# Kernel optimization log

Hardware: AMD Instinct MI355X
Metric: run time of the kernel (lower is better)

Reference implementation:

```python
import jax, jax.numpy as jnp
import numpy as np

VOXEL_SIZE = 0.04
M = 32768            # voxels surviving from previous level
V = 9                # views per fragment
C = 24               # image feature channels at finest scale
H, W = 120, 160      # fine feature map size (640x480 images /4)
C_PRE = 50           # channels[1] + tsdf + occ from previous level
UP_OFFSETS = np.array([[0,0,0,0],[0,1,0,0],[0,0,1,0],[0,0,0,1],
                       [0,1,1,0],[0,1,0,1],[0,0,1,1],[0,1,1,1]], dtype=np.int32)


def setup_inputs():
    key = jax.random.key(0)
    ks = jax.random.split(key, 10)
    pre_feat = jax.random.normal(ks[0], (M, C_PRE), jnp.float32)
    xyz = jax.random.randint(ks[1], (M, 3), 0, 94).astype(jnp.int32)
    pre_coords = jnp.concatenate([jnp.zeros((M, 1), jnp.int32), xyz], axis=1)
    feats = jax.random.normal(ks[2], (V, 1, C, H, W), jnp.float32)
    # plausible pinhole KRcam = K @ [R|t], identity rotation, jittered translation
    fx = fy = 100.0
    cx, cy = (W - 1) / 2.0, (H - 1) / 2.0
    K = np.array([[fx, 0, cx, 0], [0, fy, cy, 0], [0, 0, 1, 0], [0, 0, 0, 1]], np.float32)
    t = np.asarray(jax.random.uniform(ks[3], (V, 3), minval=-0.2, maxval=0.2))
    RT = np.tile(np.eye(4, dtype=np.float32), (V, 1, 1))
    RT[:, :3, 3] = t
    KRcam = jnp.asarray(np.einsum('ij,vjk->vik', K, RT).astype(np.float32))[:, None]  # (V,1,4,4)
    vol_origin = jnp.array([[-1.9, -1.9, 0.5]], jnp.float32)
    w2ac = jnp.asarray(np.eye(4, dtype=np.float32)[None]) + 0.01 * jax.random.normal(ks[4], (1, 4, 4), jnp.float32)
    W_sp = jax.random.normal(ks[5], (C + 1 + C_PRE, 24), jnp.float32) * 0.1
    b_sp = jnp.zeros((24,), jnp.float32)
    W_t = jax.random.normal(ks[6], (24, 1), jnp.float32) * 0.1
    b_t = jnp.zeros((1,), jnp.float32)
    W_o = jax.random.normal(ks[7], (24, 1), jnp.float32) * 0.1
    b_o = jnp.zeros((1,), jnp.float32)
    return dict(pre_feat=pre_feat, pre_coords=pre_coords, feats=feats, KRcam=KRcam,
                vol_origin=vol_origin, world_to_aligned_camera=w2ac,
                W_sp=W_sp, b_sp=b_sp, W_t=W_t, b_t=b_t, W_o=W_o, b_o=b_o)


def upsample(pre_feat, pre_coords, interval):
    # 1 -> 8 octree coordinate upsample (NeuConHead.upsample)
    off = jnp.asarray(UP_OFFSETS) * interval          # batch col stays 0
    up_coords = (pre_coords[:, None, :] + off[None]).reshape(-1, 4)
    up_feat = jnp.broadcast_to(pre_feat[:, None, :], (pre_feat.shape[0], 8, pre_feat.shape[1])).reshape(-1, pre_feat.shape[1])
    return up_feat, up_coords


def back_project(coords_xyz, origin, voxel_size, feats, KRcam):
    # coords_xyz: (N,3) int voxel coords; feats: (V,C,H,W); KRcam: (V,4,4)
    n = coords_xyz.shape[0]
    world = coords_xyz.astype(jnp.float32) * voxel_size + origin          # (N,3)
    homog = jnp.concatenate([world, jnp.ones((n, 1), jnp.float32)], 1)    # (N,4)
    im_p = jnp.einsum('vij,nj->vin', KRcam, homog)                        # (V,4,N)
    im_x, im_y, im_z = im_p[:, 0], im_p[:, 1], im_p[:, 2]
    safe_z = jnp.where(jnp.abs(im_z) > 1e-9, im_z, 1e-9)
    px = im_x / safe_z
    py = im_y / safe_z
    mask = (px >= 0) & (px <= W - 1) & (py >= 0) & (py <= H - 1) & (im_z > 0)  # (V,N)

    def sample_view(img, x, y, m):
        # bilinear grid_sample, align_corners=True, zero padding; img (C,H,W)
        x0 = jnp.floor(x); y0 = jnp.floor(y)
        wx = x - x0; wy = y - y0
        def gather(xi, yi):
            ok = (xi >= 0) & (xi < W) & (yi >= 0) & (yi < H)
            v = img[:, jnp.clip(yi, 0, H - 1).astype(jnp.int32), jnp.clip(xi, 0, W - 1).astype(jnp.int32)]
            return v * ok  # (C,N)
        top = gather(x0, y0) * (1 - wx) + gather(x0 + 1, y0) * wx
        bot = gather(x0, y0 + 1) * (1 - wx) + gather(x0 + 1, y0 + 1) * wx
        return jnp.where(m, top * (1 - wy) + bot * wy, 0.0)  # (C,N)

    fsamp = jax.vmap(sample_view)(feats, px, py, mask)        # (V,C,N)
    zed = jnp.where(mask, im_z, 0.0)                          # (V,N)
    count = mask.sum(0).astype(jnp.float32)                   # (N,)
    denom = jnp.maximum(count, 1.0)
    features = fsamp.sum(0) / denom                           # (C,N)
    z = zed.sum(0) / denom                                    # (N,)
    pos = z > 0
    npos = jnp.maximum(pos.sum(), 1).astype(jnp.float32)
    zmean = jnp.where(pos, z, 0.0).sum() / npos
    znorm = jnp.sqrt(jnp.where(pos, (z - zmean) ** 2, 0.0).sum()) + 1e-5  # torch.norm
    zn = jnp.where(pos, (z - zmean) / znorm, 0.0)
    volume = jnp.concatenate([features.T, zn[:, None]], axis=1)  # (N, C+1)
    return volume, count


def reference(pre_feat, feats, KRcam, vol_origin, world_to_aligned_camera,
              W_sp, b_sp, W_t, b_t, W_o, b_o, pre_coords):
    up_feat, up_coords = upsample(pre_feat, pre_coords, 1)
    volume, count = back_project(up_coords[:, 1:], vol_origin[0], VOXEL_SIZE,
                                 feats[:, 0], KRcam[:, 0])
    feat = jnp.concatenate([volume, up_feat], axis=1)          # (N, 75)
    # r_coords: world -> aligned camera frame (bs=1)
    world = up_coords[:, 1:].astype(jnp.float32) * VOXEL_SIZE + vol_origin[0]
    homog = jnp.concatenate([world, jnp.ones_like(world[:, :1])], axis=1)
    cam = homog @ world_to_aligned_camera[0, :3, :].T          # (N,3)
    r_coords = jnp.concatenate([cam, up_coords[:, :1].astype(jnp.float32)], axis=1)
    h = jax.nn.relu(feat @ W_sp + b_sp)                        # SPVCNN stand-in head
    tsdf = h @ W_t + b_t
    occ = h @ W_o + b_o
    out = jnp.concatenate([tsdf, occ], axis=1)                 # (N,2)
    return out, count, r_coords
```

## Files before the change

### kernel.cpp

```cpp
#include <hip/hip_runtime.h>
#include <hip/hip_fp16.h>

#define Mpts 32768
#define Vv 9
#define Cc 24
#define Hh 120
#define Ww 160
#define Npts (Mpts * 8)
#define PIX (Hh * Ww)
#define VOXEL 0.04f

#define NSLOT 64

#define OFF_TF    (NSLOT * 64)
#define OFF_PREH  (OFF_TF + Vv * PIX * 32)
#define OFF_HP    (OFF_PREH + Mpts * Cc * 4)
#define OFF_Z     (OFF_HP + Npts * Cc * 2)

typedef __attribute__((ext_vector_type(2))) float f32x2;
typedef __attribute__((ext_vector_type(4))) float f32x4;
typedef __attribute__((ext_vector_type(4))) int i32x4;

__device__ __forceinline__ unsigned pack2h(float a, float b) {
  __half2 h = __floats2half2_rn(a, b);
  return *(unsigned*)&h;
}

__device__ __forceinline__ unsigned pack4fp8(float a, float b, float c,
                                             float d) {
  int u = __builtin_amdgcn_cvt_pk_fp8_f32(a, b, 0, false);
  u = __builtin_amdgcn_cvt_pk_fp8_f32(c, d, u, true);
  return (unsigned)u;
}

__global__ __launch_bounds__(256) void prep_kernel(
    const float* __restrict__ feats, const float* __restrict__ pre_feat,
    const float* __restrict__ W_sp, const float* __restrict__ b_sp,
    uint4* __restrict__ tf, float* __restrict__ pre_h,
    double* __restrict__ red) {
  __shared__ float tile[64][Cc + 1];
  __shared__ float Wl[50 * Cc];
  __shared__ float bl[Cc];
  int blk = blockIdx.x;
  if (blk == 0) {
    red[threadIdx.x] = 0.0;
    red[threadIdx.x + 256] = 0.0;
  }

  if (blk < Vv * 300) {
    int v = blk / 300;
    int p0 = (blk % 300) * 64;
    const float* src = feats + (size_t)v * (Cc * PIX);
    for (int i = threadIdx.x; i < Cc * 64; i += 256) {
      int c = i >> 6, p = i & 63;
      tile[p][c] = src[c * PIX + p0 + p];
    }
    __syncthreads();
    uint4* dst = tf + ((size_t)v * PIX + p0) * 2;
    if (threadIdx.x < 128) {
      int p = threadIdx.x >> 1, sel = threadIdx.x & 1;
      const float* t = &tile[p][0];
      uint4 u;
      if (sel == 0) {
        u.x = pack4fp8(t[0], t[1], t[2], t[3]);
        u.y = pack4fp8(t[4], t[5], t[6], t[7]);
        u.z = pack4fp8(t[8], t[9], t[10], t[11]);
        u.w = pack4fp8(t[12], t[13], t[14], t[15]);
      } else {
        u.x = pack4fp8(t[16], t[17], t[18], t[19]);
        u.y = pack4fp8(t[20], t[21], t[22], t[23]);
        u.z = 0;
        u.w = 0;
      }
      dst[p * 2 + sel] = u;
    }
  } else {
    int mb = blk - Vv * 300;
    for (int i = threadIdx.x; i < 50 * Cc; i += 256) Wl[i] = W_sp[25 * Cc + i];
    if (threadIdx.x < Cc) bl[threadIdx.x] = b_sp[threadIdx.x];
    __syncthreads();
    int m = mb * 256 + threadIdx.x;
    float acc[Cc];
#pragma unroll
    for (int j = 0; j < Cc; j++) acc[j] = bl[j];
    const f32x2* pf = (const f32x2*)(pre_feat + (size_t)m * 50);
#pragma unroll 5
    for (int k = 0; k < 25; k++) {
      f32x2 x = __builtin_nontemporal_load(pf + k);
#pragma unroll
      for (int j = 0; j < Cc; j++)
        acc[j] += x.x * Wl[(2 * k) * Cc + j] + x.y * Wl[(2 * k + 1) * Cc + j];
    }
    f32x4* o4 = (f32x4*)(pre_h + (size_t)m * Cc);
#pragma unroll
    for (int t = 0; t < 6; t++) {
      f32x4 v4 = {acc[4 * t], acc[4 * t + 1], acc[4 * t + 2], acc[4 * t + 3]};
      __builtin_nontemporal_store(v4, o4 + t);
    }
  }
}

__device__ __forceinline__ void acc16(uint4 A, float w, float* acc) {
#pragma unroll
  for (int t = 0; t < 4; t++) {
    unsigned u = ((const unsigned*)&A)[t];
    f32x2 f0 = __builtin_amdgcn_cvt_pk_f32_fp8((int)u, false);
    f32x2 f1 = __builtin_amdgcn_cvt_pk_f32_fp8((int)u, true);
    acc[4 * t + 0] += w * f0.x;
    acc[4 * t + 1] += w * f0.y;
    acc[4 * t + 2] += w * f1.x;
    acc[4 * t + 3] += w * f1.y;
  }
}
__device__ __forceinline__ void acc8v(unsigned ux, unsigned uy, float w,
                                      float* acc) {
  f32x2 f0 = __builtin_amdgcn_cvt_pk_f32_fp8((int)ux, false);
  f32x2 f1 = __builtin_amdgcn_cvt_pk_f32_fp8((int)ux, true);
  f32x2 f2 = __builtin_amdgcn_cvt_pk_f32_fp8((int)uy, false);
  f32x2 f3 = __builtin_amdgcn_cvt_pk_f32_fp8((int)uy, true);
  acc[0] += w * f0.x;
  acc[1] += w * f0.y;
  acc[2] += w * f1.x;
  acc[3] += w * f1.y;
  acc[4] += w * f2.x;
  acc[5] += w * f2.y;
  acc[6] += w * f3.x;
  acc[7] += w * f3.y;
}

__global__ __launch_bounds__(256) void main_kernel(
    const int* __restrict__ pre_coords, const uint4* __restrict__ tfq,
    const float* __restrict__ KRcam, const float* __restrict__ vol_origin,
    const float* __restrict__ w2ac, const float* __restrict__ W_sp,
    const float* __restrict__ pre_h, float* __restrict__ out,
    unsigned* __restrict__ hp, float* __restrict__ zbuf,
    double* __restrict__ red) {
  __shared__ float KR[Vv * 12];
  __shared__ float w2a[12];
  __shared__ float orig[3];
  __shared__ float redl[3][4];
  for (int i = threadIdx.x; i < Vv * 12; i += 256) {
    int v = i / 12, r = i - v * 12;
    KR[i] = KRcam[v * 16 + r];
  }
  if (threadIdx.x < 12) w2a[threadIdx.x] = w2ac[threadIdx.x];
  if (threadIdx.x < 3) orig[threadIdx.x] = vol_origin[threadIdx.x];
  __syncthreads();

  int n = blockIdx.x * 256 + threadIdx.x;
  int m = n >> 3, o = n & 7;
  i32x4 pc = __builtin_nontemporal_load((const i32x4*)pre_coords + m);
  int cx = pc.y + ((0xB2 >> o) & 1);
  int cy = pc.z + ((0xD4 >> o) & 1);
  int cz = pc.w + ((0xE8 >> o) & 1);
  float wx0 = (float)cx * VOXEL + orig[0];
  float wy0 = (float)cy * VOXEL + orig[1];
  float wz0 = (float)cz * VOXEL + orig[2];

  {
    float camx = w2a[0] * wx0 + w2a[1] * wy0 + w2a[2] * wz0 + w2a[3];
    float camy = w2a[4] * wx0 + w2a[5] * wy0 + w2a[6] * wz0 + w2a[7];
    float camz = w2a[8] * wx0 + w2a[9] * wy0 + w2a[10] * wz0 + w2a[11];
    f32x4 rc = {camx, camy, camz, (float)pc.x};
    __builtin_nontemporal_store(rc, (f32x4*)(out + 3 * (size_t)Npts) + n);
  }

  float acc[Cc];
#pragma unroll
  for (int c = 0; c < Cc; c++) acc[c] = 0.f;
  float zsum = 0.f;
  int cnt = 0;

  for (int v = 0; v < Vv; v++) {
    const float* kr = &KR[v * 12];
    float ix = kr[0] * wx0 + kr[1] * wy0 + kr[2] * wz0 + kr[3];
    float iy = kr[4] * wx0 + kr[5] * wy0 + kr[6] * wz0 + kr[7];
    float iz = kr[8] * wx0 + kr[9] * wy0 + kr[10] * wz0 + kr[11];
    float sz = (fabsf(iz) > 1e-9f) ? iz : 1e-9f;
    float px = ix / sz;
    float py = iy / sz;
    bool msk = (px >= 0.f) && (px <= (float)(Ww - 1)) && (py >= 0.f) &&
               (py <= (float)(Hh - 1)) && (iz > 0.f);
    if (msk) {
      int x0 = (int)floorf(px), y0 = (int)floorf(py);
      int xs = min(x0, Ww - 2), ys = min(y0, Hh - 2);
      float wx = px - (float)xs, wy = py - (float)ys;
      float w00 = (1.f - wx) * (1.f - wy);
      float w10 = wx * (1.f - wy);
      float w01 = (1.f - wx) * wy;
      float w11 = wx * wy;
      const uint4* p = tfq + ((size_t)(v * PIX + ys * Ww + xs)) * 2;
      const uint4* q = p + Ww * 2;
      uint4 A = p[0], B = p[2], C = q[0], D = q[2];
      uint2 Ab = *(const uint2*)(p + 1), Bb = *(const uint2*)(p + 3);
      uint2 Cb = *(const uint2*)(q + 1), Db = *(const uint2*)(q + 3);
      acc16(A, w00, &acc[0]);
      acc8v(Ab.x, Ab.y, w00, &acc[16]);
      acc16(B, w10, &acc[0]);
      acc8v(Bb.x, Bb.y, w10, &acc[16]);
      acc16(C, w01, &acc[0]);
      acc8v(Cb.x, Cb.y, w01, &acc[16]);
      acc16(D, w11, &acc[0]);
      acc8v(Db.x, Db.y, w11, &acc[16]);
      zsum += iz;
      cnt++;
    }
  }

  float denom = fmaxf((float)cnt, 1.f);
  float invd = 1.f / denom;
  float z = zsum * invd;

  float h[Cc];
  {
    const f32x4* ph4 = (const f32x4*)(pre_h + (size_t)m * Cc);
#pragma unroll
    for (int t = 0; t < 6; t++) {
      f32x4 v4 = __builtin_nontemporal_load(ph4 + t);
      h[4 * t + 0] = v4.x;
      h[4 * t + 1] = v4.y;
      h[4 * t + 2] = v4.z;
      h[4 * t + 3] = v4.w;
    }
  }
#pragma unroll
  for (int c = 0; c < Cc; c++) {
    float f = acc[c] * invd;
#pragma unroll
    for (int j = 0; j < Cc; j++) h[j] += f * W_sp[c * Cc + j];
  }
#pragma unroll
  for (int j2 = 0; j2 < 12; j2++)
    __builtin_nontemporal_store(pack2h(h[2 * j2], h[2 * j2 + 1]),
                                hp + (size_t)j2 * Npts + n);

  __builtin_nontemporal_store(z, zbuf + n);
  __builtin_nontemporal_store((float)cnt, out + 2 * (size_t)Npts + n);

  float rz = (z > 0.f) ? z : 0.f;
  float rz2 = rz * rz;
  float rcn = (z > 0.f) ? 1.f : 0.f;
#pragma unroll
  for (int off = 32; off > 0; off >>= 1) {
    rz += __shfl_down(rz, off);
    rz2 += __shfl_down(rz2, off);
    rcn += __shfl_down(rcn, off);
  }
  int wid = threadIdx.x >> 6, lid = threadIdx.x & 63;
  if (lid == 0) {
    redl[0][wid] = rz;
    redl[1][wid] = rz2;
    redl[2][wid] = rcn;
  }
  __syncthreads();
  if (threadIdx.x == 0) {
    float a = 0.f, b = 0.f, c = 0.f;
#pragma unroll
    for (int w = 0; w < 4; w++) {
      a += redl[0][w];
      b += redl[1][w];
      c += redl[2][w];
    }
    double* slot = red + (size_t)(blockIdx.x & (NSLOT - 1)) * 8;
    atomicAdd(&slot[0], (double)a);
    atomicAdd(&slot[1], (double)b);
    atomicAdd(&slot[2], (double)c);
  }
}

__global__ __launch_bounds__(256) void final_kernel(
    const float* __restrict__ zbuf, const unsigned* __restrict__ hp,
    const float* __restrict__ W_sp, const float* __restrict__ W_t,
    const float* __restrict__ b_t, const float* __restrict__ W_o,
    const float* __restrict__ b_o, const double* __restrict__ red,
    float* __restrict__ out) {
  __shared__ float wz[Cc], wt[Cc], wo[Cc];
  __shared__ float bt, bo, s_zmean, s_izn;
  if (threadIdx.x < Cc) {
    wz[threadIdx.x] = W_sp[24 * Cc + threadIdx.x];
    wt[threadIdx.x] = W_t[threadIdx.x];
    wo[threadIdx.x] = W_o[threadIdx.x];
  }
  if (threadIdx.x == 64) {
    bt = b_t[0];
    bo = b_o[0];
  }
  if (threadIdx.x < NSLOT) {
    double a = red[(size_t)threadIdx.x * 8 + 0];
    double b = red[(size_t)threadIdx.x * 8 + 1];
    double c = red[(size_t)threadIdx.x * 8 + 2];
#pragma unroll
    for (int off = 32; off > 0; off >>= 1) {
      a += __shfl_down(a, off);
      b += __shfl_down(b, off);
      c += __shfl_down(c, off);
    }
    if (threadIdx.x == 0) {
      double npos = (c > 0.0) ? c : 1.0;
      double zmean = a / npos;
      double var = b - 2.0 * zmean * a + c * zmean * zmean;
      if (var < 0.0) var = 0.0;
      double znorm = sqrt(var) + 1e-5;
      s_zmean = (float)zmean;
      s_izn = (float)(1.0 / znorm);
    }
  }
  __syncthreads();
  int n = blockIdx.x * 256 + threadIdx.x;
  float z = __builtin_nontemporal_load(zbuf + n);
  float zn = (z > 0.f) ? (z - s_zmean) * s_izn : 0.f;
  float tsdf = bt, occ = bo;
#pragma unroll
  for (int j2 = 0; j2 < 12; j2++) {
    unsigned u = __builtin_nontemporal_load(hp + (size_t)j2 * Npts + n);
    float2 f = __half22float2(*(const __half2*)&u);
    float h0 = fmaxf(f.x + zn * wz[2 * j2], 0.f);
    float h1 = fmaxf(f.y + zn * wz[2 * j2 + 1], 0.f);
    tsdf += h0 * wt[2 * j2] + h1 * wt[2 * j2 + 1];
    occ += h0 * wo[2 * j2] + h1 * wo[2 * j2 + 1];
  }
  f32x2 o2 = {tsdf, occ};
  __builtin_nontemporal_store(o2, (f32x2*)out + n);
}

extern "C" void kernel_launch(void* const* d_in, const int* in_sizes, int n_in,
                              void* d_out, int out_size, void* d_ws,
                              size_t ws_size, hipStream_t stream) {
  const float* pre_feat = (const float*)d_in[0];
  const int* pre_coords = (const int*)d_in[1];
  const float* feats = (const float*)d_in[2];
  const float* KRcam = (const float*)d_in[3];
  const float* vol_origin = (const float*)d_in[4];
  const float* w2ac = (const float*)d_in[5];
  const float* W_sp = (const float*)d_in[6];
  const float* b_sp = (const float*)d_in[7];
  const float* W_t = (const float*)d_in[8];
  const float* b_t = (const float*)d_in[9];
  const float* W_o = (const float*)d_in[10];
  const float* b_o = (const float*)d_in[11];

  float* out = (float*)d_out;
  char* ws = (char*)d_ws;
  double* red = (double*)ws;
  uint4* tf = (uint4*)(ws + OFF_TF);
  float* pre_h = (float*)(ws + OFF_PREH);
  unsigned* hp = (unsigned*)(ws + OFF_HP);
  float* zbuf = (float*)(ws + OFF_Z);

  prep_kernel<<<Vv * 300 + Mpts / 256, 256, 0, stream>>>(feats, pre_feat, W_sp,
                                                         b_sp, tf, pre_h, red);
  main_kernel<<<Npts / 256, 256, 0, stream>>>(pre_coords, tf, KRcam,
                                              vol_origin, w2ac, W_sp, pre_h,
                                              out, hp, zbuf, red);
  final_kernel<<<Npts / 256, 256, 0, stream>>>(zbuf, hp, W_sp, W_t, b_t, W_o,
                                               b_o, red, out);
}
```

Before: 144.2 us.

## Precompute depth statistics in prep kernel and fuse final head into main kernel

```diff
diff --git a/kernel.cpp b/kernel.cpp
--- a/kernel.cpp
+++ b/kernel.cpp
@@ -10,21 +10,16 @@
 #define PIX (Hh * Ww)
 #define VOXEL 0.04f
 
-#define NSLOT 64
-
-#define OFF_TF    (NSLOT * 64)
+#define NB_TF   (Vv * 300)
+#define NB_GEMM (Mpts / 256)
+#define NB_Z    (Npts / 256)
+
+#define OFF_TF    32768
 #define OFF_PREH  (OFF_TF + Vv * PIX * 32)
-#define OFF_HP    (OFF_PREH + Mpts * Cc * 4)
-#define OFF_Z     (OFF_HP + Npts * Cc * 2)
 
 typedef __attribute__((ext_vector_type(2))) float f32x2;
 typedef __attribute__((ext_vector_type(4))) float f32x4;
 typedef __attribute__((ext_vector_type(4))) int i32x4;
-
-__device__ __forceinline__ unsigned pack2h(float a, float b) {
-  __half2 h = __floats2half2_rn(a, b);
-  return *(unsigned*)&h;
-}
 
 __device__ __forceinline__ unsigned pack4fp8(float a, float b, float c,
                                              float d) {
@@ -36,24 +31,24 @@
 __global__ __launch_bounds__(256) void prep_kernel(
     const float* __restrict__ feats, const float* __restrict__ pre_feat,
     const float* __restrict__ W_sp, const float* __restrict__ b_sp,
-    uint4* __restrict__ tf, float* __restrict__ pre_h,
-    double* __restrict__ red) {
+    const int* __restrict__ pre_coords, const float* __restrict__ KRcam,
+    const float* __restrict__ vol_origin, uint4* __restrict__ tf,
+    float* __restrict__ pre_h, double* __restrict__ red) {
   __shared__ float tile[64][Cc + 1];
   __shared__ float Wl[50 * Cc];
   __shared__ float bl[Cc];
+  __shared__ float KRs[Vv * 12];
+  __shared__ float origs[3];
+  __shared__ float redl[3][4];
   int blk = blockIdx.x;
-  if (blk == 0) {
-    red[threadIdx.x] = 0.0;
-    red[threadIdx.x + 256] = 0.0;
-  }
-
-  if (blk < Vv * 300) {
+
+  if (blk < NB_TF) {
     int v = blk / 300;
     int p0 = (blk % 300) * 64;
     const float* src = feats + (size_t)v * (Cc * PIX);
     for (int i = threadIdx.x; i < Cc * 64; i += 256) {
       int c = i >> 6, p = i & 63;
-      tile[p][c] = src[c * PIX + p0 + p];
+      tile[p][c] = __builtin_nontemporal_load(src + c * PIX + p0 + p);
     }
     __syncthreads();
     uint4* dst = tf + ((size_t)v * PIX + p0) * 2;
@@ -74,8 +69,8 @@
       }
       dst[p * 2 + sel] = u;
     }
-  } else {
-    int mb = blk - Vv * 300;
+  } else if (blk < NB_TF + NB_GEMM) {
+    int mb = blk - NB_TF;
     for (int i = threadIdx.x; i < 50 * Cc; i += 256) Wl[i] = W_sp[25 * Cc + i];
     if (threadIdx.x < Cc) bl[threadIdx.x] = b_sp[threadIdx.x];
     __syncthreads();
@@ -95,7 +90,72 @@
 #pragma unroll
     for (int t = 0; t < 6; t++) {
       f32x4 v4 = {acc[4 * t], acc[4 * t + 1], acc[4 * t + 2], acc[4 * t + 3]};
-      __builtin_nontemporal_store(v4, o4 + t);
+      o4[t] = v4;
+    }
+  } else {
+    int zblk = blk - (NB_TF + NB_GEMM);
+    for (int i = threadIdx.x; i < Vv * 12; i += 256) {
+      int v = i / 12, r = i - v * 12;
+      KRs[i] = KRcam[v * 16 + r];
+    }
+    if (threadIdx.x < 3) origs[threadIdx.x] = vol_origin[threadIdx.x];
+    __syncthreads();
+    int n = zblk * 256 + threadIdx.x;
+    int m = n >> 3, o = n & 7;
+    i32x4 pc = __builtin_nontemporal_load((const i32x4*)pre_coords + m);
+    int cx = pc.y + ((0xB2 >> o) & 1);
+    int cy = pc.z + ((0xD4 >> o) & 1);
+    int cz = pc.w + ((0xE8 >> o) & 1);
+    float wx0 = (float)cx * VOXEL + origs[0];
+    float wy0 = (float)cy * VOXEL + origs[1];
+    float wz0 = (float)cz * VOXEL + origs[2];
+    float zsum = 0.f;
+    int cnt = 0;
+    for (int v = 0; v < Vv; v++) {
+      const float* kr = &KRs[v * 12];
+      float ix = kr[0] * wx0 + kr[1] * wy0 + kr[2] * wz0 + kr[3];
+      float iy = kr[4] * wx0 + kr[5] * wy0 + kr[6] * wz0 + kr[7];
+      float iz = kr[8] * wx0 + kr[9] * wy0 + kr[10] * wz0 + kr[11];
+      float sz = (fabsf(iz) > 1e-9f) ? iz : 1e-9f;
+      float px = ix / sz;
+      float py = iy / sz;
+      bool msk = (px >= 0.f) && (px <= (float)(Ww - 1)) && (py >= 0.f) &&
+                 (py <= (float)(Hh - 1)) && (iz > 0.f);
+      if (msk) {
+        zsum += iz;
+        cnt++;
+      }
+    }
+    float denom = fmaxf((float)cnt, 1.f);
+    float z = zsum / denom;
+    float rz = (z > 0.f) ? z : 0.f;
+    float rz2 = rz * rz;
+    float rcn = (z > 0.f) ? 1.f : 0.f;
+#pragma unroll
+    for (int off = 32; off > 0; off >>= 1) {
+      rz += __shfl_down(rz, off);
+      rz2 += __shfl_down(rz2, off);
+      rcn += __shfl_down(rcn, off);
+    }
+    int wid = threadIdx.x >> 6, lid = threadIdx.x & 63;
+    if (lid == 0) {
+      redl[0][wid] = rz;
+      redl[1][wid] = rz2;
+      redl[2][wid] = rcn;
+    }
+    __syncthreads();
+    if (threadIdx.x == 0) {
+      float a = 0.f, b = 0.f, c = 0.f;
+#pragma unroll
+      for (int w = 0; w < 4; w++) {
+        a += redl[0][w];
+        b += redl[1][w];
+        c += redl[2][w];
+      }
+      double* r3 = red + (size_t)zblk * 3;
+      r3[0] = (double)a;
+      r3[1] = (double)b;
+      r3[2] = (double)c;
     }
   }
 }
@@ -132,19 +192,60 @@
     const int* __restrict__ pre_coords, const uint4* __restrict__ tfq,
     const float* __restrict__ KRcam, const float* __restrict__ vol_origin,
     const float* __restrict__ w2ac, const float* __restrict__ W_sp,
+    const float* __restrict__ W_t, const float* __restrict__ b_t,
+    const float* __restrict__ W_o, const float* __restrict__ b_o,
     const float* __restrict__ pre_h, float* __restrict__ out,
-    unsigned* __restrict__ hp, float* __restrict__ zbuf,
-    double* __restrict__ red) {
+    const double* __restrict__ red) {
   __shared__ float KR[Vv * 12];
   __shared__ float w2a[12];
   __shared__ float orig[3];
-  __shared__ float redl[3][4];
+  __shared__ double dredl[3][4];
+  __shared__ float s_zmean, s_izn;
   for (int i = threadIdx.x; i < Vv * 12; i += 256) {
     int v = i / 12, r = i - v * 12;
     KR[i] = KRcam[v * 16 + r];
   }
   if (threadIdx.x < 12) w2a[threadIdx.x] = w2ac[threadIdx.x];
   if (threadIdx.x < 3) orig[threadIdx.x] = vol_origin[threadIdx.x];
+
+  {
+    double a = 0.0, b = 0.0, c = 0.0;
+    for (int s = threadIdx.x; s < NB_Z; s += 256) {
+      const double* r3 = red + (size_t)s * 3;
+      a += r3[0];
+      b += r3[1];
+      c += r3[2];
+    }
+#pragma unroll
+    for (int off = 32; off > 0; off >>= 1) {
+      a += __shfl_down(a, off);
+      b += __shfl_down(b, off);
+      c += __shfl_down(c, off);
+    }
+    int wid = threadIdx.x >> 6, lid = threadIdx.x & 63;
+    if (lid == 0) {
+      dredl[0][wid] = a;
+      dredl[1][wid] = b;
+      dredl[2][wid] = c;
+    }
+    __syncthreads();
+    if (threadIdx.x == 0) {
+      double A = 0.0, B = 0.0, C = 0.0;
+#pragma unroll
+      for (int w = 0; w < 4; w++) {
+        A += dredl[0][w];
+        B += dredl[1][w];
+        C += dredl[2][w];
+      }
+      double npos = (C > 0.0) ? C : 1.0;
+      double zmean = A / npos;
+      double var = B - 2.0 * zmean * A + C * zmean * zmean;
+      if (var < 0.0) var = 0.0;
+      double znorm = sqrt(var) + 1e-5;
+      s_zmean = (float)zmean;
+      s_izn = (float)(1.0 / znorm);
+    }
+  }
   __syncthreads();
 
   int n = blockIdx.x * 256 + threadIdx.x;
@@ -216,7 +317,7 @@
     const f32x4* ph4 = (const f32x4*)(pre_h + (size_t)m * Cc);
 #pragma unroll
     for (int t = 0; t < 6; t++) {
-      f32x4 v4 = __builtin_nontemporal_load(ph4 + t);
+      f32x4 v4 = ph4[t];
       h[4 * t + 0] = v4.x;
       h[4 * t + 1] = v4.y;
       h[4 * t + 2] = v4.z;
@@ -229,98 +330,18 @@
 #pragma unroll
     for (int j = 0; j < Cc; j++) h[j] += f * W_sp[c * Cc + j];
   }
-#pragma unroll
-  for (int j2 = 0; j2 < 12; j2++)
-    __builtin_nontemporal_store(pack2h(h[2 * j2], h[2 * j2 + 1]),
-                                hp + (size_t)j2 * Npts + n);
-
-  __builtin_nontemporal_store(z, zbuf + n);
-  __builtin_nontemporal_store((float)cnt, out + 2 * (size_t)Npts + n);
-
-  float rz = (z > 0.f) ? z : 0.f;
-  float rz2 = rz * rz;
-  float rcn = (z > 0.f) ? 1.f : 0.f;
-#pragma unroll
-  for (int off = 32; off > 0; off >>= 1) {
-    rz += __shfl_down(rz, off);
-    rz2 += __shfl_down(rz2, off);
-    rcn += __shfl_down(rcn, off);
-  }
-  int wid = threadIdx.x >> 6, lid = threadIdx.x & 63;
-  if (lid == 0) {
-    redl[0][wid] = rz;
-    redl[1][wid] = rz2;
-    redl[2][wid] = rcn;
-  }
-  __syncthreads();
-  if (threadIdx.x == 0) {
-    float a = 0.f, b = 0.f, c = 0.f;
-#pragma unroll
-    for (int w = 0; w < 4; w++) {
-      a += redl[0][w];
-      b += redl[1][w];
-      c += redl[2][w];
-    }
-    double* slot = red + (size_t)(blockIdx.x & (NSLOT - 1)) * 8;
-    atomicAdd(&slot[0], (double)a);
-    atomicAdd(&slot[1], (double)b);
-    atomicAdd(&slot[2], (double)c);
-  }
-}
-
-__global__ __launch_bounds__(256) void final_kernel(
-    const float* __restrict__ zbuf, const unsigned* __restrict__ hp,
-    const float* __restrict__ W_sp, const float* __restrict__ W_t,
-    const float* __restrict__ b_t, const float* __restrict__ W_o,
-    const float* __restrict__ b_o, const double* __restrict__ red,
-    float* __restrict__ out) {
-  __shared__ float wz[Cc], wt[Cc], wo[Cc];
-  __shared__ float bt, bo, s_zmean, s_izn;
-  if (threadIdx.x < Cc) {
-    wz[threadIdx.x] = W_sp[24 * Cc + threadIdx.x];
-    wt[threadIdx.x] = W_t[threadIdx.x];
-    wo[threadIdx.x] = W_o[threadIdx.x];
-  }
-  if (threadIdx.x == 64) {
-    bt = b_t[0];
-    bo = b_o[0];
-  }
-  if (threadIdx.x < NSLOT) {
-    double a = red[(size_t)threadIdx.x * 8 + 0];
-    double b = red[(size_t)threadIdx.x * 8 + 1];
-    double c = red[(size_t)threadIdx.x * 8 + 2];
-#pragma unroll
-    for (int off = 32; off > 0; off >>= 1) {
-      a += __shfl_down(a, off);
-      b += __shfl_down(b, off);
-      c += __shfl_down(c, off);
-    }
-    if (threadIdx.x == 0) {
-      double npos = (c > 0.0) ? c : 1.0;
-      double zmean = a / npos;
-      double var = b - 2.0 * zmean * a + c * zmean * zmean;
-      if (var < 0.0) var = 0.0;
-      double znorm = sqrt(var) + 1e-5;
-      s_zmean = (float)zmean;
-      s_izn = (float)(1.0 / znorm);
-    }
-  }
-  __syncthreads();
-  int n = blockIdx.x * 256 + threadIdx.x;
-  float z = __builtin_nontemporal_load(zbuf + n);
+
   float zn = (z > 0.f) ? (z - s_zmean) * s_izn : 0.f;
-  float tsdf = bt, occ = bo;
-#pragma unroll
-  for (int j2 = 0; j2 < 12; j2++) {
-    unsigned u = __builtin_nontemporal_load(hp + (size_t)j2 * Npts + n);
-    float2 f = __half22float2(*(const __half2*)&u);
-    float h0 = fmaxf(f.x + zn * wz[2 * j2], 0.f);
-    float h1 = fmaxf(f.y + zn * wz[2 * j2 + 1], 0.f);
-    tsdf += h0 * wt[2 * j2] + h1 * wt[2 * j2 + 1];
-    occ += h0 * wo[2 * j2] + h1 * wo[2 * j2 + 1];
+  float tsdf = b_t[0], occ = b_o[0];
+#pragma unroll
+  for (int j = 0; j < Cc; j++) {
+    float hj = fmaxf(h[j] + zn * W_sp[24 * Cc + j], 0.f);
+    tsdf += hj * W_t[j];
+    occ += hj * W_o[j];
   }
   f32x2 o2 = {tsdf, occ};
   __builtin_nontemporal_store(o2, (f32x2*)out + n);
+  __builtin_nontemporal_store((float)cnt, out + 2 * (size_t)Npts + n);
 }
 
 extern "C" void kernel_launch(void* const* d_in, const int* in_sizes, int n_in,
@@ -344,14 +365,11 @@
   double* red = (double*)ws;
   uint4* tf = (uint4*)(ws + OFF_TF);
   float* pre_h = (float*)(ws + OFF_PREH);
-  unsigned* hp = (unsigned*)(ws + OFF_HP);
-  float* zbuf = (float*)(ws + OFF_Z);
-
-  prep_kernel<<<Vv * 300 + Mpts / 256, 256, 0, stream>>>(feats, pre_feat, W_sp,
-                                                         b_sp, tf, pre_h, red);
-  main_kernel<<<Npts / 256, 256, 0, stream>>>(pre_coords, tf, KRcam,
-                                              vol_origin, w2ac, W_sp, pre_h,
-                                              out, hp, zbuf, red);
-  final_kernel<<<Npts / 256, 256, 0, stream>>>(zbuf, hp, W_sp, W_t, b_t, W_o,
-                                               b_o, red, out);
-}
+
+  prep_kernel<<<NB_TF + NB_GEMM + NB_Z, 256, 0, stream>>>(
+      feats, pre_feat, W_sp, b_sp, pre_coords, KRcam, vol_origin, tf, pre_h,
+      red);
+  main_kernel<<<NB_Z, 256, 0, stream>>>(pre_coords, tf, KRcam, vol_origin,
+                                        w2ac, W_sp, W_t, b_t, W_o, b_o, pre_h,
+                                        out, red);
+}
```

Result: no change. 141.5 us (-1.8%).
